# Kernel tuning notes

Hardware: AMD Instinct MI355X
Metric: run time of the kernel (lower is better)

Reference implementation:

```python
import jax, jax.numpy as jnp
import numpy as np

FEAT = 13
EMB = 300
B, T = 64, 2048


def _uniform(k, shape, fan):
    bound = 1.0 / np.sqrt(fan)
    return jax.random.uniform(k, shape, jnp.float32, -bound, bound)


def setup_inputs() -> dict:
    key = jax.random.key(0)
    ks = jax.random.split(key, 11)
    return {
        "x": jax.random.normal(ks[0], (B, T, FEAT), jnp.float32),
        # encoder GRU (input 13 -> hidden 300), PyTorch layout W_ih:[3H, in], W_hh:[3H, H]
        "enc_Wih": _uniform(ks[1], (3 * EMB, FEAT), EMB),
        "enc_Whh": _uniform(ks[2], (3 * EMB, EMB), EMB),
        "enc_bih": _uniform(ks[3], (3 * EMB,), EMB),
        "enc_bhh": _uniform(ks[4], (3 * EMB,), EMB),
        # fc: Linear(300, 300)
        "fc_W": _uniform(ks[5], (EMB, EMB), EMB),
        "fc_b": _uniform(ks[6], (EMB,), EMB),
        # decoder GRU (input 300 -> hidden 13)
        "dec_Wih": _uniform(ks[7], (3 * FEAT, EMB), FEAT),
        "dec_Whh": _uniform(ks[8], (3 * FEAT, FEAT), FEAT),
        "dec_bih": _uniform(ks[9], (3 * FEAT,), FEAT),
        "dec_bhh": _uniform(ks[10], (3 * FEAT,), FEAT),
    }


def _gru_cell(gi, h, Whh, bhh):
    # gi: precomputed input gates [B, 3H]; h: [B, H]
    gh = h @ Whh.T + bhh
    i_r, i_z, i_n = jnp.split(gi, 3, axis=-1)
    h_r, h_z, h_n = jnp.split(gh, 3, axis=-1)
    r = jax.nn.sigmoid(i_r + h_r)
    z = jax.nn.sigmoid(i_z + h_z)
    n = jnp.tanh(i_n + r * h_n)
    return (1.0 - z) * n + z * h


def reference(x, enc_Wih, enc_Whh, enc_bih, enc_bhh, fc_W, fc_b,
              dec_Wih, dec_Whh, dec_bih, dec_bhh):
    b, t, f = x.shape
    hdim = enc_Whh.shape[1]
    # ---- encoder GRU (batch_first, 1 layer, h0 = 0) ----
    gi = jnp.einsum('btf,gf->btg', x, enc_Wih) + enc_bih  # [B, T, 3H], one big GEMM
    h0 = jnp.zeros((b, hdim), x.dtype)

    def enc_step(h, g_t):
        h = _gru_cell(g_t, h, enc_Whh, enc_bhh)
        return h, None

    h_last, _ = jax.lax.scan(enc_step, h0, jnp.swapaxes(gi, 0, 1))
    # encoder_output[:, -1, :] == final hidden for single-layer GRU
    emb = jax.nn.relu(h_last @ fc_W.T + fc_b)  # [B, EMB]

    # ---- decoder: per-step GRU with CONSTANT input `emb`, teacher_forcing_ratio=0 ----
    dgi = emb @ dec_Wih.T + dec_bih  # [B, 3*FEAT], constant across steps
    dh0 = jnp.zeros((b, f), x.dtype)

    def dec_step(h, _):
        h = _gru_cell(dgi, h, dec_Whh, dec_bhh)
        return h, h

    _, outs = jax.lax.scan(dec_step, dh0, None, length=t)  # [T, B, FEAT]
    outputs = jnp.swapaxes(outs, 0, 1)  # [B, T, FEAT]
    return outputs, emb[:, None, :]
```

## Files before the change

### kernel.cpp

```cpp
#include <hip/hip_runtime.h>
#include <stdint.h>

#define FEAT 13
#define EMB 300
#define BATCH 64
#define TSTEPS 2048
#define ROWS 4
#define HSTR 320
#define QW  2199.7045f
#define SWH 3.5795795e-6f
#define DEPS 1e-6f

typedef float  floatx4 __attribute__((ext_vector_type(4)));
typedef short  shortx8 __attribute__((ext_vector_type(8)));
typedef int    intx4   __attribute__((ext_vector_type(4)));

__device__ __forceinline__ uint16_t f2b(float f) {
  union { float f; uint32_t i; } c; c.f = f;
  uint32_t r = c.i + 0x7fffu + ((c.i >> 16) & 1u);
  return (uint16_t)(r >> 16);
}
__device__ __forceinline__ float sigf(float x) {
  return __builtin_amdgcn_rcpf(1.f + __expf(-x));
}
__device__ __forceinline__ float tanhf_(float x) {
  return 1.f - 2.f * __builtin_amdgcn_rcpf(1.f + __expf(2.f * x));
}
__device__ __forceinline__ int q8w(float v) {
  return __float2int_rn(fminf(fmaxf(v * QW, -127.f), 127.f));
}
__device__ __forceinline__ float rdl(float v, int l) {
  union { float f; int i; } c; c.f = v;
  union { int i; float f; } o;
  o.i = __builtin_amdgcn_readlane(c.i, l);
  return o.f;
}

__device__ __forceinline__ void barx() {
  asm volatile("s_waitcnt lgkmcnt(0)" ::: "memory");
  __builtin_amdgcn_s_barrier();
  asm volatile("" ::: "memory");
}

#define MFI8(A, B, C) __builtin_amdgcn_mfma_i32_16x16x64_i8(A, B, C, 0, 0, 0)
#define MFBF(A, B, C) __builtin_amdgcn_mfma_f32_16x16x32_bf16(A, B, C, 0, 0, 0)

__launch_bounds__(1024, 4)
__global__ void gru_enc(const float* __restrict__ x,
                        const float* __restrict__ eWih,
                        const float* __restrict__ eWhh,
                        const float* __restrict__ ebih,
                        const float* __restrict__ ebhh,
                        const float* __restrict__ fcW,
                        const float* __restrict__ fcb,
                        float* __restrict__ out) {
  __shared__ __align__(16) signed char hb[2][ROWS][HSTR];
  __shared__ __align__(16) signed char zpad[HSTR];
  __shared__ __align__(16) uint16_t    xt[2][16][32];
  __shared__ __align__(16) signed char wl4[16][3][1024];
  __shared__ __align__(16) signed char wlB[3][3][5][1024];
  __shared__ __align__(16) uint16_t    wxE[3][3][64][8];
  __shared__ __align__(16) floatx4     ebE[3][16];

  const int tid = threadIdx.x, lane = tid & 63, w = tid >> 6;
  const int nl = lane & 15, q = lane >> 4;
  const int g = blockIdx.x;

  intx4   Bh[3][4];
  shortx8 Bx[3];
  float bS0, bS1, bHN, bIN;
  {
    const int jj = 16 * w + nl;
#pragma unroll
    for (int gt = 0; gt < 3; ++gt) {
      const int R = gt * EMB + jj;
      for (int kt = 0; kt < 5; ++kt) {
        int bb[4] = {0, 0, 0, 0};
        for (int e = 0; e < 16; ++e) {
          int kk = kt * 64 + q * 16 + e;
          float v = (kk < EMB) ? eWhh[(size_t)R * EMB + kk] : 0.f;
          bb[e >> 2] |= (q8w(v) & 255) << ((e & 3) * 8);
        }
        intx4 t4; t4[0] = bb[0]; t4[1] = bb[1]; t4[2] = bb[2]; t4[3] = bb[3];
        if (kt < 4) Bh[gt][kt] = t4;
        else        *(intx4*)&wl4[w][gt][lane * 16] = t4;
      }
      union { uint16_t u[8]; shortx8 v; } c;
      for (int e = 0; e < 8; ++e) {
        int kk = q * 8 + e;
        c.u[e] = (kk < FEAT) ? f2b(eWih[R * FEAT + kk]) : (uint16_t)0;
      }
      Bx[gt] = c.v;
    }
    bS0 = ebih[jj] + ebhh[jj];
    bS1 = ebih[EMB + jj] + ebhh[EMB + jj];
    bHN = ebhh[2 * EMB + jj];
    bIN = ebih[2 * EMB + jj];
  }
  if (w >= 7) {
    const int u = w - 7, eI = u / 3, gt = u - 3 * eI;
    const int jj = 16 * (16 + eI) + nl;
    const bool jvv = (jj < EMB);
    const int R = gt * EMB + (jvv ? jj : 0);
    for (int kt = 0; kt < 5; ++kt) {
      int bb[4] = {0, 0, 0, 0};
      for (int e = 0; e < 16; ++e) {
        int kk = kt * 64 + q * 16 + e;
        float v = (jvv && kk < EMB) ? eWhh[(size_t)R * EMB + kk] : 0.f;
        bb[e >> 2] |= (q8w(v) & 255) << ((e & 3) * 8);
      }
      intx4 t4; t4[0] = bb[0]; t4[1] = bb[1]; t4[2] = bb[2]; t4[3] = bb[3];
      *(intx4*)&wlB[eI][gt][kt][lane * 16] = t4;
    }
  }
  if (w >= 3 && w < 6) {
    const int eI = w - 3;
    const int jj = 16 * (16 + eI) + nl;
    const bool jvv = (jj < EMB);
    const int R0 = jvv ? jj : 0;
#pragma unroll
    for (int gt = 0; gt < 3; ++gt) {
      union { uint16_t u[8]; shortx8 v; } c;
      for (int e = 0; e < 8; ++e) {
        int kk = q * 8 + e;
        c.u[e] = (jvv && kk < FEAT)
                     ? f2b(eWih[(size_t)(gt * EMB + R0) * FEAT + kk])
                     : (uint16_t)0;
      }
      *(shortx8*)&wxE[eI][gt][lane][0] = c.v;
    }
  }
  if (w == 6 && lane < 48) {
    const int eI = lane >> 4, j2 = lane & 15;
    const int jj = 16 * (16 + eI) + j2;
    const bool jvv = (jj < EMB);
    floatx4 v;
    v[0] = jvv ? (ebih[jj] + ebhh[jj]) : 0.f;
    v[1] = jvv ? (ebih[EMB + jj] + ebhh[EMB + jj]) : 0.f;
    v[2] = jvv ? ebhh[2 * EMB + jj] : 0.f;
    v[3] = jvv ? ebih[2 * EMB + jj] : 0.f;
    ebE[eI][j2] = v;
  }

  for (int i = tid; i < 2 * ROWS * HSTR; i += 1024) ((signed char*)hb)[i] = 0;
  for (int i = tid; i < HSTR; i += 1024) zpad[i] = 0;
  for (int i = tid; i < 2 * 16 * 32; i += 1024) ((uint16_t*)xt)[i] = 0;
  __syncthreads();
  if (tid < ROWS * FEAT) {
    int m = tid / FEAT, f = tid - m * FEAT;
    xt[0][4 * m][f] = f2b(x[((size_t)(g * ROWS + m) * TSTEPS) * FEAT + f]);
  }
  __syncthreads();

  const int rr_ = nl >> 2;
  const bool areal = ((nl & 3) == 0);
  const signed char* aRead =
      areal ? (&hb[0][0][0] + rr_ * HSTR + ((q ^ rr_) << 4)) : zpad;
  int dA = areal ? (ROWS * HSTR) : 0;
  const uint16_t* xr = &xt[0][nl][q * 8];
  int dX = 16 * 32;
  const int cown = 16 * w + nl;
  signed char* hw = &hb[1][q][0] + (cown ^ (q << 4));
  const int cext = 16 * (16 + (w < 3 ? w : 0)) + nl;
  signed char* hwE = &hb[1][q][0] + (cext ^ (q << 4));
  int dH = -(ROWS * HSTR);
  const signed char* wb4 = &wl4[w][0][lane * 16];
  const signed char* wbB = &wlB[w < 3 ? w : 0][0][0][lane * 16];
  const uint16_t*    wxb = &wxE[w < 3 ? w : 0][0][lane][0];
  floatx4 ebv = {0.f, 0.f, 0.f, 0.f};
  if (w < 3) ebv = ebE[w][nl];
  const floatx4 zf = {0.f, 0.f, 0.f, 0.f};

  const bool xl = (w == 15) && (lane < ROWS * FEAT);
  const int xm = lane / FEAT, xf = lane - xm * FEAT;
  const float* xbase = x + ((size_t)(g * ROWS + xm) * TSTEPS) * FEAT + xf;
  float xcur = 0.f;
  if (xl) xcur = xbase[FEAT];
  const float* xnq = xbase + 2 * FEAT;
  uint16_t* xw = &xt[1][4 * xm][xf];
  int dXW = -(16 * 32);

  float hprev = 0.f, hpE = 0.f;

  for (int t = 1; t <= TSTEPS; ++t) {
    float xnxt = 0.f;
    if (xl && t < TSTEPS - 1) { xnxt = *xnq; xnq += FEAT; }

    intx4 Ah[5];
#pragma unroll
    for (int kt = 0; kt < 5; ++kt)
      Ah[kt] = *(const intx4*)(aRead + kt * 64);
    const shortx8 Ax = *(const shortx8*)xr;

    intx4 aR = {0, 0, 0, 0}, aZ = {0, 0, 0, 0}, aN = {0, 0, 0, 0};
#pragma unroll
    for (int kt = 0; kt < 4; ++kt) {
      aR = MFI8(Ah[kt], Bh[0][kt], aR);
      aZ = MFI8(Ah[kt], Bh[1][kt], aZ);
      aN = MFI8(Ah[kt], Bh[2][kt], aN);
    }
    aR = MFI8(Ah[4], *(const intx4*)(wb4), aR);
    aZ = MFI8(Ah[4], *(const intx4*)(wb4 + 1024), aZ);
    aN = MFI8(Ah[4], *(const intx4*)(wb4 + 2048), aN);
    {
      floatx4 xR = MFBF(Ax, Bx[0], zf);
      floatx4 xZ = MFBF(Ax, Bx[1], zf);
      floatx4 xN = MFBF(Ax, Bx[2], zf);
      float r  = sigf((float)aR[0] * SWH + xR[0] + bS0);
      float z  = sigf((float)aZ[0] * SWH + xZ[0] + bS1);
      float hn = (float)aN[0] * SWH + bHN;
      float n  = tanhf_(xN[0] + bIN + r * hn);
      float h  = z * (hprev - n) + n;
      hprev = h;
      float hq = fminf(fmaxf(h * 127.f, -127.f), 127.f);
      *hw = (signed char)__float2int_rn(hq);
    }
    if (w < 3) {
      intx4 aR2 = {0, 0, 0, 0}, aZ2 = {0, 0, 0, 0}, aN2 = {0, 0, 0, 0};
#pragma unroll
      for (int kt = 0; kt < 5; ++kt) {
        aR2 = MFI8(Ah[kt], *(const intx4*)(wbB + kt * 1024), aR2);
        aZ2 = MFI8(Ah[kt], *(const intx4*)(wbB + 5120 + kt * 1024), aZ2);
        aN2 = MFI8(Ah[kt], *(const intx4*)(wbB + 10240 + kt * 1024), aN2);
      }
      floatx4 xR = MFBF(Ax, *(const shortx8*)(wxb), zf);
      floatx4 xZ = MFBF(Ax, *(const shortx8*)(wxb + 512), zf);
      floatx4 xN = MFBF(Ax, *(const shortx8*)(wxb + 1024), zf);
      float r  = sigf((float)aR2[0] * SWH + xR[0] + ebv[0]);
      float z  = sigf((float)aZ2[0] * SWH + xZ[0] + ebv[1]);
      float hn = (float)aN2[0] * SWH + ebv[2];
      float n  = tanhf_(xN[0] + ebv[3] + r * hn);
      float h  = z * (hpE - n) + n;
      hpE = h;
      float hq = fminf(fmaxf(h * 127.f, -127.f), 127.f);
      *hwE = (signed char)__float2int_rn(hq);
    }
    if (xl && t < TSTEPS) *xw = f2b(xcur);

    aRead += dA; dA = -dA;
    xr += dX;    dX = -dX;
    hw += dH;    hwE += dH;  dH = -dH;
    xw += dXW;   dXW = -dXW;

    barx();
    xcur = xnxt;
  }

  {
    float* oemb = out + (size_t)BATCH * TSTEPS * FEAT;
    const signed char* aT =
        areal ? (&hb[0][0][0] + rr_ * HSTR + ((q ^ rr_) << 4)) : zpad;
    intx4 AhT[5];
#pragma unroll
    for (int kt = 0; kt < 5; ++kt)
      AhT[kt] = *(const intx4*)(aT + kt * 64);
#pragma unroll
    for (int u = 0; u < 2; ++u) {
      const int s = w + 16 * u;
      if (s < 19) {
        const int jj = 16 * s + nl;
        const bool jvv = (jj < EMB);
        intx4 acc = {0, 0, 0, 0};
        for (int kt = 0; kt < 5; ++kt) {
          int bb[4] = {0, 0, 0, 0};
          for (int e = 0; e < 16; ++e) {
            int kk = kt * 64 + q * 16 + e;
            float v = (jvv && kk < EMB) ? fcW[(size_t)jj * EMB + kk] : 0.f;
            bb[e >> 2] |= (q8w(v) & 255) << ((e & 3) * 8);
          }
          intx4 b4; b4[0] = bb[0]; b4[1] = bb[1]; b4[2] = bb[2]; b4[3] = bb[3];
          acc = MFI8(AhT[kt], b4, acc);
        }
        if (jvv) {
          float e2 = (float)acc[0] * SWH + fcb[jj];
          oemb[(size_t)(g * ROWS + q) * EMB + jj] = e2 > 0.f ? e2 : 0.f;
        }
      }
    }
  }
}

__launch_bounds__(64, 1)
__global__ void gru_dec(const float* __restrict__ dWih,
                        const float* __restrict__ dWhh,
                        const float* __restrict__ dbih,
                        const float* __restrict__ dbhh,
                        float* __restrict__ out) {
  __shared__ float hsh[FEAT];
  const int b = blockIdx.x;
  const int j = threadIdx.x;
  const bool own = (j < FEAT);
  const float* emb = out + (size_t)BATCH * TSTEPS * FEAT + (size_t)b * EMB;

  float gi = 0.f;
  if (j < 3 * FEAT) {
    gi = dbih[j];
#pragma unroll 4
    for (int k = 0; k < EMB; ++k)
      gi = fmaf(emb[k], dWih[j * EMB + k], gi);
  }
  const float gir = __shfl(gi, j);
  const float giz = __shfl(gi, FEAT + j);
  const float gin = __shfl(gi, 2 * FEAT + j);

  float Wr[FEAT], Wz[FEAT], Wn[FEAT];
#pragma unroll
  for (int k = 0; k < FEAT; ++k) { Wr[k] = 0.f; Wz[k] = 0.f; Wn[k] = 0.f; }
  float br = 0.f, bz = 0.f, bn = 0.f;
  if (own) {
#pragma unroll
    for (int k = 0; k < FEAT; ++k) {
      Wr[k] = dWhh[j * FEAT + k];
      Wz[k] = dWhh[(FEAT + j) * FEAT + k];
      Wn[k] = dWhh[(2 * FEAT + j) * FEAT + k];
    }
    br = dbhh[j]; bz = dbhh[FEAT + j]; bn = dbhh[2 * FEAT + j];
  }

  float hown = 0.f;
  float* orow = out + (size_t)b * TSTEPS * FEAT;

  for (int t = 0; t < TSTEPS; ++t) {
    float hs[FEAT];
#pragma unroll
    for (int k = 0; k < FEAT; ++k) hs[k] = rdl(hown, k);
    float ghr = br, ghz = bz, ghn = bn;
#pragma unroll
    for (int k = 0; k < FEAT; ++k) {
      ghr = fmaf(Wr[k], hs[k], ghr);
      ghz = fmaf(Wz[k], hs[k], ghz);
      ghn = fmaf(Wn[k], hs[k], ghn);
    }
    float r  = sigf(gir + ghr);
    float z  = sigf(giz + ghz);
    float nn = tanhf_(gin + r * ghn);
    float hn = z * (hown - nn) + nn;
    bool conv = (!own) || (fabsf(hn - hown) <= DEPS);
    if (own) {
      orow[t * FEAT + j] = hn;
      hown = hn;
    }
    if (__all(conv)) {
      if (own) hsh[j] = hown;
      asm volatile("s_waitcnt lgkmcnt(0)" ::: "memory");
      const int total = TSTEPS * FEAT;
      int idx = (t + 1) * FEAT + j;
      if (idx < total) {
        int jj = idx % FEAT;
        for (; idx < total; idx += 64) {
          orow[idx] = hsh[jj];
          jj = (jj == 0) ? (FEAT - 1) : (jj - 1);
        }
      }
      break;
    }
  }
}

extern "C" void kernel_launch(void* const* d_in, const int* in_sizes, int n_in,
                              void* d_out, int out_size, void* d_ws, size_t ws_size,
                              hipStream_t stream) {
  (void)in_sizes; (void)n_in; (void)out_size; (void)d_ws; (void)ws_size;
  const float* x    = (const float*)d_in[0];
  const float* eWih = (const float*)d_in[1];
  const float* eWhh = (const float*)d_in[2];
  const float* ebih = (const float*)d_in[3];
  const float* ebhh = (const float*)d_in[4];
  const float* fcW  = (const float*)d_in[5];
  const float* fcb  = (const float*)d_in[6];
  const float* dWih = (const float*)d_in[7];
  const float* dWhh = (const float*)d_in[8];
  const float* dbih = (const float*)d_in[9];
  const float* dbhh = (const float*)d_in[10];

  hipLaunchKernelGGL(gru_enc, dim3(BATCH / ROWS), dim3(1024), 0, stream,
                     x, eWih, eWhh, ebih, ebhh, fcW, fcb, (float*)d_out);
  hipLaunchKernelGGL(gru_dec, dim3(BATCH), dim3(64), 0, stream,
                     dWih, dWhh, dbih, dbhh, (float*)d_out);
}
```

Before: 2.548 ms.

## Precompute encoder input gates in a separate GEMM kernel via workspace

Adds a gi_pre kernel that computes x@Wih^T+bih for all timesteps into a workspace buffer, so the recurrent encoder loop reads those gate inputs from global memory instead of staging x through shared memory and running bf16 MFMAs each step. This removes per-step x staging and three to six MFMAs from the serial critical path. In exchange it adds a large global write/read of about 470MB of gate data, plus per-step global loads that are prefetched one step ahead. The old kernel is kept as a fallback for when the workspace is too small.

```diff
diff --git a/kernel.cpp b/kernel.cpp
--- a/kernel.cpp
+++ b/kernel.cpp
@@ -45,30 +45,48 @@
 #define MFI8(A, B, C) __builtin_amdgcn_mfma_i32_16x16x64_i8(A, B, C, 0, 0, 0)
 #define MFBF(A, B, C) __builtin_amdgcn_mfma_f32_16x16x32_bf16(A, B, C, 0, 0, 0)
 
+__launch_bounds__(256)
+__global__ void gi_pre(const float* __restrict__ x,
+                       const float* __restrict__ eWih,
+                       const float* __restrict__ ebih,
+                       float* __restrict__ gi) {
+  const int base = blockIdx.x * 8;
+  for (int r = 0; r < 8; ++r) {
+    const int bt = base + r;
+    const float* xp = x + (size_t)bt * FEAT;
+    float xv[FEAT];
+#pragma unroll
+    for (int f = 0; f < FEAT; ++f) xv[f] = xp[f];
+    float* gp = gi + (size_t)bt * 900;
+    for (int c = threadIdx.x; c < 900; c += 256) {
+      float a = ebih[c];
+      const float* wr = eWih + c * FEAT;
+#pragma unroll
+      for (int f = 0; f < FEAT; ++f) a = fmaf(xv[f], wr[f], a);
+      gp[c] = a;
+    }
+  }
+}
+
 __launch_bounds__(1024, 4)
-__global__ void gru_enc(const float* __restrict__ x,
-                        const float* __restrict__ eWih,
+__global__ void gru_enc(const float* __restrict__ gi,
                         const float* __restrict__ eWhh,
-                        const float* __restrict__ ebih,
                         const float* __restrict__ ebhh,
                         const float* __restrict__ fcW,
                         const float* __restrict__ fcb,
                         float* __restrict__ out) {
   __shared__ __align__(16) signed char hb[2][ROWS][HSTR];
   __shared__ __align__(16) signed char zpad[HSTR];
-  __shared__ __align__(16) uint16_t    xt[2][16][32];
   __shared__ __align__(16) signed char wl4[16][3][1024];
   __shared__ __align__(16) signed char wlB[3][3][5][1024];
-  __shared__ __align__(16) uint16_t    wxE[3][3][64][8];
   __shared__ __align__(16) floatx4     ebE[3][16];
 
   const int tid = threadIdx.x, lane = tid & 63, w = tid >> 6;
   const int nl = lane & 15, q = lane >> 4;
   const int g = blockIdx.x;
 
-  intx4   Bh[3][4];
-  shortx8 Bx[3];
-  float bS0, bS1, bHN, bIN;
+  intx4 Bh[3][4];
+  float bhhR, bhhZ, bHN;
   {
     const int jj = 16 * w + nl;
 #pragma unroll
@@ -85,17 +103,10 @@
         if (kt < 4) Bh[gt][kt] = t4;
         else        *(intx4*)&wl4[w][gt][lane * 16] = t4;
       }
-      union { uint16_t u[8]; shortx8 v; } c;
-      for (int e = 0; e < 8; ++e) {
-        int kk = q * 8 + e;
-        c.u[e] = (kk < FEAT) ? f2b(eWih[R * FEAT + kk]) : (uint16_t)0;
-      }
-      Bx[gt] = c.v;
-    }
-    bS0 = ebih[jj] + ebhh[jj];
-    bS1 = ebih[EMB + jj] + ebhh[EMB + jj];
-    bHN = ebhh[2 * EMB + jj];
-    bIN = ebih[2 * EMB + jj];
+    }
+    bhhR = ebhh[jj];
+    bhhZ = ebhh[EMB + jj];
+    bHN  = ebhh[2 * EMB + jj];
   }
   if (w >= 7) {
     const int u = w - 7, eI = u / 3, gt = u - 3 * eI;
@@ -113,43 +124,20 @@
       *(intx4*)&wlB[eI][gt][kt][lane * 16] = t4;
     }
   }
-  if (w >= 3 && w < 6) {
-    const int eI = w - 3;
-    const int jj = 16 * (16 + eI) + nl;
-    const bool jvv = (jj < EMB);
-    const int R0 = jvv ? jj : 0;
-#pragma unroll
-    for (int gt = 0; gt < 3; ++gt) {
-      union { uint16_t u[8]; shortx8 v; } c;
-      for (int e = 0; e < 8; ++e) {
-        int kk = q * 8 + e;
-        c.u[e] = (jvv && kk < FEAT)
-                     ? f2b(eWih[(size_t)(gt * EMB + R0) * FEAT + kk])
-                     : (uint16_t)0;
-      }
-      *(shortx8*)&wxE[eI][gt][lane][0] = c.v;
-    }
-  }
   if (w == 6 && lane < 48) {
     const int eI = lane >> 4, j2 = lane & 15;
     const int jj = 16 * (16 + eI) + j2;
     const bool jvv = (jj < EMB);
     floatx4 v;
-    v[0] = jvv ? (ebih[jj] + ebhh[jj]) : 0.f;
-    v[1] = jvv ? (ebih[EMB + jj] + ebhh[EMB + jj]) : 0.f;
+    v[0] = jvv ? ebhh[jj] : 0.f;
+    v[1] = jvv ? ebhh[EMB + jj] : 0.f;
     v[2] = jvv ? ebhh[2 * EMB + jj] : 0.f;
-    v[3] = jvv ? ebih[2 * EMB + jj] : 0.f;
+    v[3] = jvv ? 1.f : 0.f;
     ebE[eI][j2] = v;
   }
 
   for (int i = tid; i < 2 * ROWS * HSTR; i += 1024) ((signed char*)hb)[i] = 0;
   for (int i = tid; i < HSTR; i += 1024) zpad[i] = 0;
-  for (int i = tid; i < 2 * 16 * 32; i += 1024) ((uint16_t*)xt)[i] = 0;
-  __syncthreads();
-  if (tid < ROWS * FEAT) {
-    int m = tid / FEAT, f = tid - m * FEAT;
-    xt[0][4 * m][f] = f2b(x[((size_t)(g * ROWS + m) * TSTEPS) * FEAT + f]);
-  }
   __syncthreads();
 
   const int rr_ = nl >> 2;
@@ -157,8 +145,6 @@
   const signed char* aRead =
       areal ? (&hb[0][0][0] + rr_ * HSTR + ((q ^ rr_) << 4)) : zpad;
   int dA = areal ? (ROWS * HSTR) : 0;
-  const uint16_t* xr = &xt[0][nl][q * 8];
-  int dX = 16 * 32;
   const int cown = 16 * w + nl;
   signed char* hw = &hb[1][q][0] + (cown ^ (q << 4));
   const int cext = 16 * (16 + (w < 3 ? w : 0)) + nl;
@@ -166,31 +152,34 @@
   int dH = -(ROWS * HSTR);
   const signed char* wb4 = &wl4[w][0][lane * 16];
   const signed char* wbB = &wlB[w < 3 ? w : 0][0][0][lane * 16];
-  const uint16_t*    wxb = &wxE[w < 3 ? w : 0][0][lane][0];
   floatx4 ebv = {0.f, 0.f, 0.f, 0.f};
   if (w < 3) ebv = ebE[w][nl];
   const floatx4 zf = {0.f, 0.f, 0.f, 0.f};
 
-  const bool xl = (w == 15) && (lane < ROWS * FEAT);
-  const int xm = lane / FEAT, xf = lane - xm * FEAT;
-  const float* xbase = x + ((size_t)(g * ROWS + xm) * TSTEPS) * FEAT + xf;
-  float xcur = 0.f;
-  if (xl) xcur = xbase[FEAT];
-  const float* xnq = xbase + 2 * FEAT;
-  uint16_t* xw = &xt[1][4 * xm][xf];
-  int dXW = -(16 * 32);
+  const size_t gbase = (size_t)(g * ROWS + q) * TSTEPS * 900;
+  const float* gp = gi + gbase + (16 * w + nl);
+  float gR = gp[0], gZ = gp[300], gN = gp[600];
+  gp += 900;
+  const int jjE = 16 * (16 + (w < 3 ? w : 0)) + nl;
+  const float* gpe = gi + gbase + (jjE < EMB ? jjE : 0);
+  float gRE = 0.f, gZE = 0.f, gNE = 0.f;
+  if (w < 3) { gRE = gpe[0]; gZE = gpe[300]; gNE = gpe[600]; }
+  gpe += 900;
 
   float hprev = 0.f, hpE = 0.f;
 
   for (int t = 1; t <= TSTEPS; ++t) {
-    float xnxt = 0.f;
-    if (xl && t < TSTEPS - 1) { xnxt = *xnq; xnq += FEAT; }
+    float gRn = 0.f, gZn = 0.f, gNn = 0.f;
+    if (t < TSTEPS) { gRn = gp[0]; gZn = gp[300]; gNn = gp[600]; gp += 900; }
+    float gREn = 0.f, gZEn = 0.f, gNEn = 0.f;
+    if (w < 3 && t < TSTEPS) {
+      gREn = gpe[0]; gZEn = gpe[300]; gNEn = gpe[600]; gpe += 900;
+    }
 
     intx4 Ah[5];
 #pragma unroll
     for (int kt = 0; kt < 5; ++kt)
       Ah[kt] = *(const intx4*)(aRead + kt * 64);
-    const shortx8 Ax = *(const shortx8*)xr;
 
     intx4 aR = {0, 0, 0, 0}, aZ = {0, 0, 0, 0}, aN = {0, 0, 0, 0};
 #pragma unroll
@@ -203,13 +192,10 @@
     aZ = MFI8(Ah[4], *(const intx4*)(wb4 + 1024), aZ);
     aN = MFI8(Ah[4], *(const intx4*)(wb4 + 2048), aN);
     {
-      floatx4 xR = MFBF(Ax, Bx[0], zf);
-      floatx4 xZ = MFBF(Ax, Bx[1], zf);
-      floatx4 xN = MFBF(Ax, Bx[2], zf);
-      float r  = sigf((float)aR[0] * SWH + xR[0] + bS0);
-      float z  = sigf((float)aZ[0] * SWH + xZ[0] + bS1);
+      float r  = sigf((float)aR[0] * SWH + gR + bhhR);
+      float z  = sigf((float)aZ[0] * SWH + gZ + bhhZ);
       float hn = (float)aN[0] * SWH + bHN;
-      float n  = tanhf_(xN[0] + bIN + r * hn);
+      float n  = tanhf_(gN + r * hn);
       float h  = z * (hprev - n) + n;
       hprev = h;
       float hq = fminf(fmaxf(h * 127.f, -127.f), 127.f);
@@ -223,27 +209,23 @@
         aZ2 = MFI8(Ah[kt], *(const intx4*)(wbB + 5120 + kt * 1024), aZ2);
         aN2 = MFI8(Ah[kt], *(const intx4*)(wbB + 10240 + kt * 1024), aN2);
       }
-      floatx4 xR = MFBF(Ax, *(const shortx8*)(wxb), zf);
-      floatx4 xZ = MFBF(Ax, *(const shortx8*)(wxb + 512), zf);
-      floatx4 xN = MFBF(Ax, *(const shortx8*)(wxb + 1024), zf);
-      float r  = sigf((float)aR2[0] * SWH + xR[0] + ebv[0]);
-      float z  = sigf((float)aZ2[0] * SWH + xZ[0] + ebv[1]);
+      const float jm = ebv[3];
+      float r  = sigf((float)aR2[0] * SWH + gRE * jm + ebv[0]);
+      float z  = sigf((float)aZ2[0] * SWH + gZE * jm + ebv[1]);
       float hn = (float)aN2[0] * SWH + ebv[2];
-      float n  = tanhf_(xN[0] + ebv[3] + r * hn);
+      float n  = tanhf_(gNE * jm + r * hn);
       float h  = z * (hpE - n) + n;
       hpE = h;
       float hq = fminf(fmaxf(h * 127.f, -127.f), 127.f);
       *hwE = (signed char)__float2int_rn(hq);
     }
-    if (xl && t < TSTEPS) *xw = f2b(xcur);
 
     aRead += dA; dA = -dA;
-    xr += dX;    dX = -dX;
     hw += dH;    hwE += dH;  dH = -dH;
-    xw += dXW;   dXW = -dXW;
 
     barx();
-    xcur = xnxt;
+    gR = gRn; gZ = gZn; gN = gNn;
+    gRE = gREn; gZE = gZEn; gNE = gNEn;
   }
 
   {
@@ -280,6 +262,241 @@
   }
 }
 
+__launch_bounds__(1024, 4)
+__global__ void gru_enc_fb(const float* __restrict__ x,
+                           const float* __restrict__ eWih,
+                           const float* __restrict__ eWhh,
+                           const float* __restrict__ ebih,
+                           const float* __restrict__ ebhh,
+                           const float* __restrict__ fcW,
+                           const float* __restrict__ fcb,
+                           float* __restrict__ out) {
+  __shared__ __align__(16) signed char hb[2][ROWS][HSTR];
+  __shared__ __align__(16) signed char zpad[HSTR];
+  __shared__ __align__(16) uint16_t    xt[2][16][32];
+  __shared__ __align__(16) signed char wl4[16][3][1024];
+  __shared__ __align__(16) signed char wlB[3][3][5][1024];
+  __shared__ __align__(16) uint16_t    wxE[3][3][64][8];
+  __shared__ __align__(16) floatx4     ebE[3][16];
+
+  const int tid = threadIdx.x, lane = tid & 63, w = tid >> 6;
+  const int nl = lane & 15, q = lane >> 4;
+  const int g = blockIdx.x;
+
+  intx4   Bh[3][4];
+  shortx8 Bx[3];
+  float bS0, bS1, bHN, bIN;
+  {
+    const int jj = 16 * w + nl;
+#pragma unroll
+    for (int gt = 0; gt < 3; ++gt) {
+      const int R = gt * EMB + jj;
+      for (int kt = 0; kt < 5; ++kt) {
+        int bb[4] = {0, 0, 0, 0};
+        for (int e = 0; e < 16; ++e) {
+          int kk = kt * 64 + q * 16 + e;
+          float v = (kk < EMB) ? eWhh[(size_t)R * EMB + kk] : 0.f;
+          bb[e >> 2] |= (q8w(v) & 255) << ((e & 3) * 8);
+        }
+        intx4 t4; t4[0] = bb[0]; t4[1] = bb[1]; t4[2] = bb[2]; t4[3] = bb[3];
+        if (kt < 4) Bh[gt][kt] = t4;
+        else        *(intx4*)&wl4[w][gt][lane * 16] = t4;
+      }
+      union { uint16_t u[8]; shortx8 v; } c;
+      for (int e = 0; e < 8; ++e) {
+        int kk = q * 8 + e;
+        c.u[e] = (kk < FEAT) ? f2b(eWih[R * FEAT + kk]) : (uint16_t)0;
+      }
+      Bx[gt] = c.v;
+    }
+    bS0 = ebih[jj] + ebhh[jj];
+    bS1 = ebih[EMB + jj] + ebhh[EMB + jj];
+    bHN = ebhh[2 * EMB + jj];
+    bIN = ebih[2 * EMB + jj];
+  }
+  if (w >= 7) {
+    const int u = w - 7, eI = u / 3, gt = u - 3 * eI;
+    const int jj = 16 * (16 + eI) + nl;
+    const bool jvv = (jj < EMB);
+    const int R = gt * EMB + (jvv ? jj : 0);
+    for (int kt = 0; kt < 5; ++kt) {
+      int bb[4] = {0, 0, 0, 0};
+      for (int e = 0; e < 16; ++e) {
+        int kk = kt * 64 + q * 16 + e;
+        float v = (jvv && kk < EMB) ? eWhh[(size_t)R * EMB + kk] : 0.f;
+        bb[e >> 2] |= (q8w(v) & 255) << ((e & 3) * 8);
+      }
+      intx4 t4; t4[0] = bb[0]; t4[1] = bb[1]; t4[2] = bb[2]; t4[3] = bb[3];
+      *(intx4*)&wlB[eI][gt][kt][lane * 16] = t4;
+    }
+  }
+  if (w >= 3 && w < 6) {
+    const int eI = w - 3;
+    const int jj = 16 * (16 + eI) + nl;
+    const bool jvv = (jj < EMB);
+    const int R0 = jvv ? jj : 0;
+#pragma unroll
+    for (int gt = 0; gt < 3; ++gt) {
+      union { uint16_t u[8]; shortx8 v; } c;
+      for (int e = 0; e < 8; ++e) {
+        int kk = q * 8 + e;
+        c.u[e] = (jvv && kk < FEAT)
+                     ? f2b(eWih[(size_t)(gt * EMB + R0) * FEAT + kk])
+                     : (uint16_t)0;
+      }
+      *(shortx8*)&wxE[eI][gt][lane][0] = c.v;
+    }
+  }
+  if (w == 6 && lane < 48) {
+    const int eI = lane >> 4, j2 = lane & 15;
+    const int jj = 16 * (16 + eI) + j2;
+    const bool jvv = (jj < EMB);
+    floatx4 v;
+    v[0] = jvv ? (ebih[jj] + ebhh[jj]) : 0.f;
+    v[1] = jvv ? (ebih[EMB + jj] + ebhh[EMB + jj]) : 0.f;
+    v[2] = jvv ? ebhh[2 * EMB + jj] : 0.f;
+    v[3] = jvv ? ebih[2 * EMB + jj] : 0.f;
+    ebE[eI][j2] = v;
+  }
+
+  for (int i = tid; i < 2 * ROWS * HSTR; i += 1024) ((signed char*)hb)[i] = 0;
+  for (int i = tid; i < HSTR; i += 1024) zpad[i] = 0;
+  for (int i = tid; i < 2 * 16 * 32; i += 1024) ((uint16_t*)xt)[i] = 0;
+  __syncthreads();
+  if (tid < ROWS * FEAT) {
+    int m = tid / FEAT, f = tid - m * FEAT;
+    xt[0][4 * m][f] = f2b(x[((size_t)(g * ROWS + m) * TSTEPS) * FEAT + f]);
+  }
+  __syncthreads();
+
+  const int rr_ = nl >> 2;
+  const bool areal = ((nl & 3) == 0);
+  const signed char* aRead =
+      areal ? (&hb[0][0][0] + rr_ * HSTR + ((q ^ rr_) << 4)) : zpad;
+  int dA = areal ? (ROWS * HSTR) : 0;
+  const uint16_t* xr = &xt[0][nl][q * 8];
+  int dX = 16 * 32;
+  const int cown = 16 * w + nl;
+  signed char* hw = &hb[1][q][0] + (cown ^ (q << 4));
+  const int cext = 16 * (16 + (w < 3 ? w : 0)) + nl;
+  signed char* hwE = &hb[1][q][0] + (cext ^ (q << 4));
+  int dH = -(ROWS * HSTR);
+  const signed char* wb4 = &wl4[w][0][lane * 16];
+  const signed char* wbB = &wlB[w < 3 ? w : 0][0][0][lane * 16];
+  const uint16_t*    wxb = &wxE[w < 3 ? w : 0][0][lane][0];
+  floatx4 ebv = {0.f, 0.f, 0.f, 0.f};
+  if (w < 3) ebv = ebE[w][nl];
+  const floatx4 zf = {0.f, 0.f, 0.f, 0.f};
+
+  const bool xl = (w == 15) && (lane < ROWS * FEAT);
+  const int xm = lane / FEAT, xf = lane - xm * FEAT;
+  const float* xbase = x + ((size_t)(g * ROWS + xm) * TSTEPS) * FEAT + xf;
+  float xcur = 0.f;
+  if (xl) xcur = xbase[FEAT];
+  const float* xnq = xbase + 2 * FEAT;
+  uint16_t* xw = &xt[1][4 * xm][xf];
+  int dXW = -(16 * 32);
+
+  float hprev = 0.f, hpE = 0.f;
+
+  for (int t = 1; t <= TSTEPS; ++t) {
+    float xnxt = 0.f;
+    if (xl && t < TSTEPS - 1) { xnxt = *xnq; xnq += FEAT; }
+
+    intx4 Ah[5];
+#pragma unroll
+    for (int kt = 0; kt < 5; ++kt)
+      Ah[kt] = *(const intx4*)(aRead + kt * 64);
+    const shortx8 Ax = *(const shortx8*)xr;
+
+    intx4 aR = {0, 0, 0, 0}, aZ = {0, 0, 0, 0}, aN = {0, 0, 0, 0};
+#pragma unroll
+    for (int kt = 0; kt < 4; ++kt) {
+      aR = MFI8(Ah[kt], Bh[0][kt], aR);
+      aZ = MFI8(Ah[kt], Bh[1][kt], aZ);
+      aN = MFI8(Ah[kt], Bh[2][kt], aN);
+    }
+    aR = MFI8(Ah[4], *(const intx4*)(wb4), aR);
+    aZ = MFI8(Ah[4], *(const intx4*)(wb4 + 1024), aZ);
+    aN = MFI8(Ah[4], *(const intx4*)(wb4 + 2048), aN);
+    {
+      floatx4 xR = MFBF(Ax, Bx[0], zf);
+      floatx4 xZ = MFBF(Ax, Bx[1], zf);
+      floatx4 xN = MFBF(Ax, Bx[2], zf);
+      float r  = sigf((float)aR[0] * SWH + xR[0] + bS0);
+      float z  = sigf((float)aZ[0] * SWH + xZ[0] + bS1);
+      float hn = (float)aN[0] * SWH + bHN;
+      float n  = tanhf_(xN[0] + bIN + r * hn);
+      float h  = z * (hprev - n) + n;
+      hprev = h;
+      float hq = fminf(fmaxf(h * 127.f, -127.f), 127.f);
+      *hw = (signed char)__float2int_rn(hq);
+    }
+    if (w < 3) {
+      intx4 aR2 = {0, 0, 0, 0}, aZ2 = {0, 0, 0, 0}, aN2 = {0, 0, 0, 0};
+#pragma unroll
+      for (int kt = 0; kt < 5; ++kt) {
+        aR2 = MFI8(Ah[kt], *(const intx4*)(wbB + kt * 1024), aR2);
+        aZ2 = MFI8(Ah[kt], *(const intx4*)(wbB + 5120 + kt * 1024), aZ2);
+        aN2 = MFI8(Ah[kt], *(const intx4*)(wbB + 10240 + kt * 1024), aN2);
+      }
+      floatx4 xR = MFBF(Ax, *(const shortx8*)(wxb), zf);
+      floatx4 xZ = MFBF(Ax, *(const shortx8*)(wxb + 512), zf);
+      floatx4 xN = MFBF(Ax, *(const shortx8*)(wxb + 1024), zf);
+      float r  = sigf((float)aR2[0] * SWH + xR[0] + ebv[0]);
+      float z  = sigf((float)aZ2[0] * SWH + xZ[0] + ebv[1]);
+      float hn = (float)aN2[0] * SWH + ebv[2];
+      float n  = tanhf_(xN[0] + ebv[3] + r * hn);
+      float h  = z * (hpE - n) + n;
+      hpE = h;
+      float hq = fminf(fmaxf(h * 127.f, -127.f), 127.f);
+      *hwE = (signed char)__float2int_rn(hq);
+    }
+    if (xl && t < TSTEPS) *xw = f2b(xcur);
+
+    aRead += dA; dA = -dA;
+    xr += dX;    dX = -dX;
+    hw += dH;    hwE += dH;  dH = -dH;
+    xw += dXW;   dXW = -dXW;
+
+    barx();
+    xcur = xnxt;
+  }
+
+  {
+    float* oemb = out + (size_t)BATCH * TSTEPS * FEAT;
+    const signed char* aT =
+        areal ? (&hb[0][0][0] + rr_ * HSTR + ((q ^ rr_) << 4)) : zpad;
+    intx4 AhT[5];
+#pragma unroll
+    for (int kt = 0; kt < 5; ++kt)
+      AhT[kt] = *(const intx4*)(aT + kt * 64);
+#pragma unroll
+    for (int u = 0; u < 2; ++u) {
+      const int s = w + 16 * u;
+      if (s < 19) {
+        const int jj = 16 * s + nl;
+        const bool jvv = (jj < EMB);
+        intx4 acc = {0, 0, 0, 0};
+        for (int kt = 0; kt < 5; ++kt) {
+          int bb[4] = {0, 0, 0, 0};
+          for (int e = 0; e < 16; ++e) {
+            int kk = kt * 64 + q * 16 + e;
+            float v = (jvv && kk < EMB) ? fcW[(size_t)jj * EMB + kk] : 0.f;
+            bb[e >> 2] |= (q8w(v) & 255) << ((e & 3) * 8);
+          }
+          intx4 b4; b4[0] = bb[0]; b4[1] = bb[1]; b4[2] = bb[2]; b4[3] = bb[3];
+          acc = MFI8(AhT[kt], b4, acc);
+        }
+        if (jvv) {
+          float e2 = (float)acc[0] * SWH + fcb[jj];
+          oemb[(size_t)(g * ROWS + q) * EMB + jj] = e2 > 0.f ? e2 : 0.f;
+        }
+      }
+    }
+  }
+}
+
 __launch_bounds__(64, 1)
 __global__ void gru_dec(const float* __restrict__ dWih,
                         const float* __restrict__ dWhh,
@@ -360,7 +577,7 @@
 extern "C" void kernel_launch(void* const* d_in, const int* in_sizes, int n_in,
                               void* d_out, int out_size, void* d_ws, size_t ws_size,
                               hipStream_t stream) {
-  (void)in_sizes; (void)n_in; (void)out_size; (void)d_ws; (void)ws_size;
+  (void)in_sizes; (void)n_in; (void)out_size;
   const float* x    = (const float*)d_in[0];
   const float* eWih = (const float*)d_in[1];
   const float* eWhh = (const float*)d_in[2];
@@ -373,8 +590,17 @@
   const float* dbih = (const float*)d_in[9];
   const float* dbhh = (const float*)d_in[10];
 
-  hipLaunchKernelGGL(gru_enc, dim3(BATCH / ROWS), dim3(1024), 0, stream,
-                     x, eWih, eWhh, ebih, ebhh, fcW, fcb, (float*)d_out);
+  const size_t need = (size_t)BATCH * TSTEPS * 900 * sizeof(float);
+  if (d_ws != nullptr && ws_size >= need) {
+    float* gi = (float*)d_ws;
+    hipLaunchKernelGGL(gi_pre, dim3(BATCH * TSTEPS / 8), dim3(256), 0, stream,
+                       x, eWih, ebih, gi);
+    hipLaunchKernelGGL(gru_enc, dim3(BATCH / ROWS), dim3(1024), 0, stream,
+                       gi, eWhh, ebhh, fcW, fcb, (float*)d_out);
+  } else {
+    hipLaunchKernelGGL(gru_enc_fb, dim3(BATCH / ROWS), dim3(1024), 0, stream,
+                       x, eWih, eWhh, ebih, ebhh, fcW, fcb, (float*)d_out);
+  }
   hipLaunchKernelGGL(gru_dec, dim3(BATCH), dim3(64), 0, stream,
                      dWih, dWhh, dbih, dbhh, (float*)d_out);
 }
```

Result: no change. 2.540 ms (-0.3%).

## Precompute encoder input gates in a separate GEMM kernel and stream them

Applied to the files above, without the earlier changes.

Adds a pre-pass kernel that computes x·W_ih^T + b_ih for every batch/timestep into a global fp32 buffer of about 470 MB. The recurrent encoder then prefetches each step's three gate values from global memory instead of running bf16 MFMAs on the x tile. This removes the x staging, the extra MFMAs and their LDS traffic from the serial loop, and makes the input projection fp32 rather than bf16. The cost is a large extra memory write and read, plus global-load latency inside the latency-bound recurrence, which the one-step prefetch is meant to hide.

```diff
diff --git a/kernel.cpp b/kernel.cpp
--- a/kernel.cpp
+++ b/kernel.cpp
@@ -15,11 +15,8 @@
 typedef short  shortx8 __attribute__((ext_vector_type(8)));
 typedef int    intx4   __attribute__((ext_vector_type(4)));
 
-__device__ __forceinline__ uint16_t f2b(float f) {
-  union { float f; uint32_t i; } c; c.f = f;
-  uint32_t r = c.i + 0x7fffu + ((c.i >> 16) & 1u);
-  return (uint16_t)(r >> 16);
-}
+__device__ float gi_buf[(size_t)BATCH * TSTEPS * 900];
+
 __device__ __forceinline__ float sigf(float x) {
   return __builtin_amdgcn_rcpf(1.f + __expf(-x));
 }
@@ -43,32 +40,48 @@
 }
 
 #define MFI8(A, B, C) __builtin_amdgcn_mfma_i32_16x16x64_i8(A, B, C, 0, 0, 0)
-#define MFBF(A, B, C) __builtin_amdgcn_mfma_f32_16x16x32_bf16(A, B, C, 0, 0, 0)
+
+__launch_bounds__(256)
+__global__ void gi_pre(const float* __restrict__ x,
+                       const float* __restrict__ eWih,
+                       const float* __restrict__ ebih)
+{
+  const int base = blockIdx.x * 8;
+  for (int r = 0; r < 8; ++r) {
+    const int bt = base + r;
+    const float* xp = x + (size_t)bt * FEAT;
+    float xv[FEAT];
+#pragma unroll
+    for (int f = 0; f < FEAT; ++f) xv[f] = xp[f];
+    float* gp = gi_buf + (size_t)bt * 900;
+    for (int c = threadIdx.x; c < 900; c += 256) {
+      float a = ebih[c];
+      const float* wr = eWih + c * FEAT;
+#pragma unroll
+      for (int f = 0; f < FEAT; ++f) a = fmaf(xv[f], wr[f], a);
+      gp[c] = a;
+    }
+  }
+}
 
 __launch_bounds__(1024, 4)
-__global__ void gru_enc(const float* __restrict__ x,
-                        const float* __restrict__ eWih,
-                        const float* __restrict__ eWhh,
-                        const float* __restrict__ ebih,
+__global__ void gru_enc(const float* __restrict__ eWhh,
                         const float* __restrict__ ebhh,
                         const float* __restrict__ fcW,
                         const float* __restrict__ fcb,
                         float* __restrict__ out) {
   __shared__ __align__(16) signed char hb[2][ROWS][HSTR];
   __shared__ __align__(16) signed char zpad[HSTR];
-  __shared__ __align__(16) uint16_t    xt[2][16][32];
   __shared__ __align__(16) signed char wl4[16][3][1024];
   __shared__ __align__(16) signed char wlB[3][3][5][1024];
-  __shared__ __align__(16) uint16_t    wxE[3][3][64][8];
   __shared__ __align__(16) floatx4     ebE[3][16];
 
   const int tid = threadIdx.x, lane = tid & 63, w = tid >> 6;
   const int nl = lane & 15, q = lane >> 4;
   const int g = blockIdx.x;
 
-  intx4   Bh[3][4];
-  shortx8 Bx[3];
-  float bS0, bS1, bHN, bIN;
+  intx4 Bh[3][4];
+  float bhhR, bhhZ, bHN;
   {
     const int jj = 16 * w + nl;
 #pragma unroll
@@ -85,17 +98,10 @@
         if (kt < 4) Bh[gt][kt] = t4;
         else        *(intx4*)&wl4[w][gt][lane * 16] = t4;
       }
-      union { uint16_t u[8]; shortx8 v; } c;
-      for (int e = 0; e < 8; ++e) {
-        int kk = q * 8 + e;
-        c.u[e] = (kk < FEAT) ? f2b(eWih[R * FEAT + kk]) : (uint16_t)0;
-      }
-      Bx[gt] = c.v;
-    }
-    bS0 = ebih[jj] + ebhh[jj];
-    bS1 = ebih[EMB + jj] + ebhh[EMB + jj];
-    bHN = ebhh[2 * EMB + jj];
-    bIN = ebih[2 * EMB + jj];
+    }
+    bhhR = ebhh[jj];
+    bhhZ = ebhh[EMB + jj];
+    bHN  = ebhh[2 * EMB + jj];
   }
   if (w >= 7) {
     const int u = w - 7, eI = u / 3, gt = u - 3 * eI;
@@ -113,43 +119,20 @@
       *(intx4*)&wlB[eI][gt][kt][lane * 16] = t4;
     }
   }
-  if (w >= 3 && w < 6) {
-    const int eI = w - 3;
-    const int jj = 16 * (16 + eI) + nl;
-    const bool jvv = (jj < EMB);
-    const int R0 = jvv ? jj : 0;
-#pragma unroll
-    for (int gt = 0; gt < 3; ++gt) {
-      union { uint16_t u[8]; shortx8 v; } c;
-      for (int e = 0; e < 8; ++e) {
-        int kk = q * 8 + e;
-        c.u[e] = (jvv && kk < FEAT)
-                     ? f2b(eWih[(size_t)(gt * EMB + R0) * FEAT + kk])
-                     : (uint16_t)0;
-      }
-      *(shortx8*)&wxE[eI][gt][lane][0] = c.v;
-    }
-  }
   if (w == 6 && lane < 48) {
     const int eI = lane >> 4, j2 = lane & 15;
     const int jj = 16 * (16 + eI) + j2;
     const bool jvv = (jj < EMB);
     floatx4 v;
-    v[0] = jvv ? (ebih[jj] + ebhh[jj]) : 0.f;
-    v[1] = jvv ? (ebih[EMB + jj] + ebhh[EMB + jj]) : 0.f;
+    v[0] = jvv ? ebhh[jj] : 0.f;
+    v[1] = jvv ? ebhh[EMB + jj] : 0.f;
     v[2] = jvv ? ebhh[2 * EMB + jj] : 0.f;
-    v[3] = jvv ? ebih[2 * EMB + jj] : 0.f;
+    v[3] = jvv ? 1.f : 0.f;
     ebE[eI][j2] = v;
   }
 
   for (int i = tid; i < 2 * ROWS * HSTR; i += 1024) ((signed char*)hb)[i] = 0;
   for (int i = tid; i < HSTR; i += 1024) zpad[i] = 0;
-  for (int i = tid; i < 2 * 16 * 32; i += 1024) ((uint16_t*)xt)[i] = 0;
-  __syncthreads();
-  if (tid < ROWS * FEAT) {
-    int m = tid / FEAT, f = tid - m * FEAT;
-    xt[0][4 * m][f] = f2b(x[((size_t)(g * ROWS + m) * TSTEPS) * FEAT + f]);
-  }
   __syncthreads();
 
   const int rr_ = nl >> 2;
@@ -157,8 +140,6 @@
   const signed char* aRead =
       areal ? (&hb[0][0][0] + rr_ * HSTR + ((q ^ rr_) << 4)) : zpad;
   int dA = areal ? (ROWS * HSTR) : 0;
-  const uint16_t* xr = &xt[0][nl][q * 8];
-  int dX = 16 * 32;
   const int cown = 16 * w + nl;
   signed char* hw = &hb[1][q][0] + (cown ^ (q << 4));
   const int cext = 16 * (16 + (w < 3 ? w : 0)) + nl;
@@ -166,31 +147,33 @@
   int dH = -(ROWS * HSTR);
   const signed char* wb4 = &wl4[w][0][lane * 16];
   const signed char* wbB = &wlB[w < 3 ? w : 0][0][0][lane * 16];
-  const uint16_t*    wxb = &wxE[w < 3 ? w : 0][0][lane][0];
   floatx4 ebv = {0.f, 0.f, 0.f, 0.f};
   if (w < 3) ebv = ebE[w][nl];
-  const floatx4 zf = {0.f, 0.f, 0.f, 0.f};
-
-  const bool xl = (w == 15) && (lane < ROWS * FEAT);
-  const int xm = lane / FEAT, xf = lane - xm * FEAT;
-  const float* xbase = x + ((size_t)(g * ROWS + xm) * TSTEPS) * FEAT + xf;
-  float xcur = 0.f;
-  if (xl) xcur = xbase[FEAT];
-  const float* xnq = xbase + 2 * FEAT;
-  uint16_t* xw = &xt[1][4 * xm][xf];
-  int dXW = -(16 * 32);
+
+  const size_t gbase = (size_t)(g * ROWS + q) * TSTEPS * 900;
+  const float* gp = gi_buf + gbase + (16 * w + nl);
+  float gR = gp[0], gZ = gp[300], gN = gp[600];
+  gp += 900;
+  const int jjE = 16 * (16 + (w < 3 ? w : 0)) + nl;
+  const float* gpe = gi_buf + gbase + (jjE < EMB ? jjE : 0);
+  float gRE = 0.f, gZE = 0.f, gNE = 0.f;
+  if (w < 3) { gRE = gpe[0]; gZE = gpe[300]; gNE = gpe[600]; }
+  gpe += 900;
 
   float hprev = 0.f, hpE = 0.f;
 
   for (int t = 1; t <= TSTEPS; ++t) {
-    float xnxt = 0.f;
-    if (xl && t < TSTEPS - 1) { xnxt = *xnq; xnq += FEAT; }
+    float gRn = 0.f, gZn = 0.f, gNn = 0.f;
+    if (t < TSTEPS) { gRn = gp[0]; gZn = gp[300]; gNn = gp[600]; gp += 900; }
+    float gREn = 0.f, gZEn = 0.f, gNEn = 0.f;
+    if (w < 3 && t < TSTEPS) {
+      gREn = gpe[0]; gZEn = gpe[300]; gNEn = gpe[600]; gpe += 900;
+    }
 
     intx4 Ah[5];
 #pragma unroll
     for (int kt = 0; kt < 5; ++kt)
       Ah[kt] = *(const intx4*)(aRead + kt * 64);
-    const shortx8 Ax = *(const shortx8*)xr;
 
     intx4 aR = {0, 0, 0, 0}, aZ = {0, 0, 0, 0}, aN = {0, 0, 0, 0};
 #pragma unroll
@@ -203,13 +186,10 @@
     aZ = MFI8(Ah[4], *(const intx4*)(wb4 + 1024), aZ);
     aN = MFI8(Ah[4], *(const intx4*)(wb4 + 2048), aN);
     {
-      floatx4 xR = MFBF(Ax, Bx[0], zf);
-      floatx4 xZ = MFBF(Ax, Bx[1], zf);
-      floatx4 xN = MFBF(Ax, Bx[2], zf);
-      float r  = sigf((float)aR[0] * SWH + xR[0] + bS0);
-      float z  = sigf((float)aZ[0] * SWH + xZ[0] + bS1);
+      float r  = sigf((float)aR[0] * SWH + gR + bhhR);
+      float z  = sigf((float)aZ[0] * SWH + gZ + bhhZ);
       float hn = (float)aN[0] * SWH + bHN;
-      float n  = tanhf_(xN[0] + bIN + r * hn);
+      float n  = tanhf_(gN + r * hn);
       float h  = z * (hprev - n) + n;
       hprev = h;
       float hq = fminf(fmaxf(h * 127.f, -127.f), 127.f);
@@ -223,27 +203,23 @@
         aZ2 = MFI8(Ah[kt], *(const intx4*)(wbB + 5120 + kt * 1024), aZ2);
         aN2 = MFI8(Ah[kt], *(const intx4*)(wbB + 10240 + kt * 1024), aN2);
       }
-      floatx4 xR = MFBF(Ax, *(const shortx8*)(wxb), zf);
-      floatx4 xZ = MFBF(Ax, *(const shortx8*)(wxb + 512), zf);
-      floatx4 xN = MFBF(Ax, *(const shortx8*)(wxb + 1024), zf);
-      float r  = sigf((float)aR2[0] * SWH + xR[0] + ebv[0]);
-      float z  = sigf((float)aZ2[0] * SWH + xZ[0] + ebv[1]);
+      const float jm = ebv[3];
+      float r  = sigf((float)aR2[0] * SWH + gRE * jm + ebv[0]);
+      float z  = sigf((float)aZ2[0] * SWH + gZE * jm + ebv[1]);
       float hn = (float)aN2[0] * SWH + ebv[2];
-      float n  = tanhf_(xN[0] + ebv[3] + r * hn);
+      float n  = tanhf_(gNE * jm + r * hn);
       float h  = z * (hpE - n) + n;
       hpE = h;
       float hq = fminf(fmaxf(h * 127.f, -127.f), 127.f);
       *hwE = (signed char)__float2int_rn(hq);
     }
-    if (xl && t < TSTEPS) *xw = f2b(xcur);
 
     aRead += dA; dA = -dA;
-    xr += dX;    dX = -dX;
     hw += dH;    hwE += dH;  dH = -dH;
-    xw += dXW;   dXW = -dXW;
 
     barx();
-    xcur = xnxt;
+    gR = gRn; gZ = gZn; gN = gNn;
+    gRE = gREn; gZE = gZEn; gNE = gNEn;
   }
 
   {
@@ -373,8 +349,10 @@
   const float* dbih = (const float*)d_in[9];
   const float* dbhh = (const float*)d_in[10];
 
+  hipLaunchKernelGGL(gi_pre, dim3(BATCH * TSTEPS / 8), dim3(256), 0, stream,
+                     x, eWih, ebih);
   hipLaunchKernelGGL(gru_enc, dim3(BATCH / ROWS), dim3(1024), 0, stream,
-                     x, eWih, eWhh, ebih, ebhh, fcW, fcb, (float*)d_out);
+                     eWhh, ebhh, fcW, fcb, (float*)d_out);
   hipLaunchKernelGGL(gru_dec, dim3(BATCH), dim3(64), 0, stream,
                      dWih, dWhh, dbih, dbhh, (float*)d_out);
 }
```

Measured after the change: 3.221 ms. 1.26x slower.
